# Kernel optimization log

Measured on AMD Instinct MI355X. Metric: run time of the kernel, lower is better.

## Reference

```python
import jax, jax.numpy as jnp
import numpy as np

N = 1000   # node count forced by fc1_1 in_features=1680 (see shape derivation)
E = 8000   # edges, avg degree ~8
F_IN = 6   # node feature dim (first 3 = pos, zeroed in forward)


def setup_inputs() -> dict:
    key = jax.random.key(0)
    ks = jax.random.split(key, 24)
    f = lambda k, s, sc=1.0: jax.random.normal(k, s, dtype=jnp.float32) * sc
    inp = {
        "x": f(ks[0], (N, F_IN)),
        "edge_index": jax.random.randint(ks[1], (2, E), 0, N, dtype=jnp.int64),
        # GCNConv weights (xavier-ish scale)
        "W1": f(ks[2], (F_IN, 32), 0.4), "b1": jnp.zeros((32,), jnp.float32),
        "W2": f(ks[3], (32, 32), 0.18), "b2": jnp.zeros((32,), jnp.float32),
        # Conv2d kernels, OIHW
        "k1": f(ks[4], (3, 1, 3, 2), 0.3), "kb1": jnp.zeros((3,), jnp.float32),
        "k2": f(ks[5], (6, 3, 3, 2), 0.2), "kb2": jnp.zeros((6,), jnp.float32),
        "k3": f(ks[6], (3, 6, 3, 2), 0.2), "kb3": jnp.zeros((3,), jnp.float32),
        "k4": f(ks[7], (1, 3, 3, 2), 0.2), "kb4": jnp.zeros((1,), jnp.float32),
        # FC head (torch Linear layout: [out, in])
        "fw1": f(ks[8], (1024, 1680), 0.02), "fb1": jnp.zeros((1024,), jnp.float32),
        "fw2": f(ks[9], (1024, 1024), 0.03), "fb2": jnp.zeros((1024,), jnp.float32),
        "fw3": f(ks[10], (64, 1024), 0.03), "fb3": jnp.zeros((64,), jnp.float32),
    }
    return inp


def _conv2d(x, w, b):
    out = jax.lax.conv_general_dilated(
        x, w, window_strides=(1, 1), padding="VALID",
        dimension_numbers=("NCHW", "OIHW", "NCHW"))
    return out + b[None, :, None, None]


def _maxpool2(x):  # MaxPool2d((2,1), stride=(2,1))
    return jax.lax.reduce_window(x, -jnp.inf, jax.lax.max,
                                 (1, 1, 2, 1), (1, 1, 2, 1), "VALID")


def reference(x, edge_index, W1, b1, W2, b2, k1, kb1, k2, kb2, k3, kb3, k4, kb4,
              fw1, fb1, fw2, fb2, fw3, fb3):
    num_nodes = x.shape[0]
    # forward zeroes the first 3 features (positions)
    x = x.at[:, :3].set(0.0)

    loop = jnp.arange(num_nodes)
    row = jnp.concatenate([edge_index[0], loop])
    col = jnp.concatenate([edge_index[1], loop])
    deg = jnp.zeros((num_nodes,), x.dtype).at[col].add(1.0)
    dinv = jnp.where(deg > 0, jax.lax.rsqrt(deg), 0.0)
    norm = (dinv[row] * dinv[col])[:, None]  # [E+N, 1]

    def gcn(h, W, b):
        hw = h @ W                                   # [N, 32]
        msg = hw[row] * norm                         # gather + scale
        return jax.ops.segment_sum(msg, col, num_segments=num_nodes) + b

    leaky = lambda v: jnp.where(v > 0, v, 0.2 * v)   # LeakyReLU(0.2)
    h = leaky(gcn(x, W1, b1))
    h = leaky(gcn(h, W2, b2))                        # [N, 32]

    img = h[None, None]                              # [1, 1, N, 32]
    img = _maxpool2(jax.nn.relu(_conv2d(img, k1, kb1)))   # [1,3,499,31]
    img = _maxpool2(jax.nn.relu(_conv2d(img, k2, kb2)))   # [1,6,248,30]
    img = _maxpool2(jax.nn.relu(_conv2d(img, k3, kb3)))   # [1,3,123,29]
    img = _maxpool2(jax.nn.relu(_conv2d(img, k4, kb4)))   # [1,1,60,28]

    v = img.reshape(-1)                              # [1680]
    v = v @ fw1.T + fb1                              # no activation between FCs (as in source)
    v = v @ fw2.T + fb2
    v = v @ fw3.T + fb3                              # [64]
    return v
```

## Files before the change

kernel.cpp:

```cpp
#include <hip/hip_runtime.h>

#define LEAKY(v) ((v) > 0.0f ? (v) : 0.2f * (v))

__global__ void k1_prep(const float* __restrict__ x, const int* __restrict__ col,
                        const float* __restrict__ W1, float* __restrict__ deg,
                        float* __restrict__ aggs ,
                        float* __restrict__ xw, int n, int E) {
    int tid = blockIdx.x * blockDim.x + threadIdx.x;
    int NT = gridDim.x * blockDim.x;
    for (int i = tid; i < 2 * n * 32; i += NT) aggs[i] = 0.0f;
    for (int e = tid; e < E; e += NT) atomicAdd(&deg[col[e]], 1.0f);
    for (int t = tid; t < n * 32; t += NT) {
        int j = t & 31, nn = t >> 5;
        xw[t] = x[nn*6+3] * W1[96+j]
              + x[nn*6+4] * W1[128+j]
              + x[nn*6+5] * W1[160+j];
    }
}

__global__ void k_scatter(const float* __restrict__ xw, const float* __restrict__ deg,
                          const int* __restrict__ row, const int* __restrict__ col,
                          float* __restrict__ agg, int E, int n) {
    int tid = blockIdx.x * blockDim.x + threadIdx.x;
    int total = (E + n) * 32;
    if (tid >= total) return;
    int e = tid >> 5, j = tid & 31;
    int r, c; float nrm;
    if (e < E) {
        r = row[e]; c = col[e];
        nrm = (1.0f / sqrtf(deg[r] + 1.0f)) * (1.0f / sqrtf(deg[c] + 1.0f));
    } else {
        r = c = e - E;
        nrm = 1.0f / (deg[r] + 1.0f);
    }
    atomicAdd(&agg[c * 32 + j], xw[r * 32 + j] * nrm);
}

__global__ void k3_xw2(const float* __restrict__ agg1, const float* __restrict__ b1,
                       const float* __restrict__ W2, float* __restrict__ xw, int n) {
    int tid = blockIdx.x * blockDim.x + threadIdx.x;
    if (tid >= n * 32) return;
    int j = tid & 31, nn = tid >> 5;
    const float* a = agg1 + nn * 32;
    float s = 0.0f;
#pragma unroll
    for (int f = 0; f < 32; ++f) {
        float v = a[f] + b1[f];
        v = LEAKY(v);
        s += v * W2[f * 32 + j];
    }
    xw[tid] = s;
}

__global__ void k5_conv1(const float* __restrict__ h2, const float* __restrict__ b2,
                         const float* __restrict__ w, const float* __restrict__ bias,
                         float* __restrict__ out) {
    const int Hp = 499, Wo = 31, total = 3 * Hp * Wo;
    int t0 = blockIdx.x * blockDim.x + threadIdx.x;
    if (t0 >= total) return;
    int ow = t0 % Wo; int t = t0 / Wo; int oh = t % Hp; int co = t / Hp;
    const float* ip = h2 + (2 * oh) * 32 + ow;
    float vals[4][2];
#pragma unroll
    for (int r = 0; r < 4; ++r)
#pragma unroll
        for (int cx = 0; cx < 2; ++cx) {
            float v = ip[r * 32 + cx] + b2[ow + cx];
            vals[r][cx] = LEAKY(v);
        }
    const float* wp = w + co * 6;
    float a0 = vals[0][0]*wp[0] + vals[0][1]*wp[1] + vals[1][0]*wp[2]
             + vals[1][1]*wp[3] + vals[2][0]*wp[4] + vals[2][1]*wp[5];
    float a1 = vals[1][0]*wp[0] + vals[1][1]*wp[1] + vals[2][0]*wp[2]
             + vals[2][1]*wp[3] + vals[3][0]*wp[4] + vals[3][1]*wp[5];
    float m = fmaxf(a0, a1) + bias[co];
    out[t0] = fmaxf(m, 0.0f);
}

__global__ void k6_conv2(const float* __restrict__ in, const float* __restrict__ w,
                         const float* __restrict__ bias, float* __restrict__ out) {
    const int CI = 3, Hin = 499, Win = 31, Hp = 248, Wo = 30, total = 6 * Hp * Wo;
    int t0 = blockIdx.x * blockDim.x + threadIdx.x;
    if (t0 >= total) return;
    int ow = t0 % Wo; int t = t0 / Wo; int oh = t % Hp; int co = t / Hp;
    float a0 = 0.0f, a1 = 0.0f;
#pragma unroll
    for (int ci = 0; ci < CI; ++ci) {
        const float* q = in + (ci * Hin + 2 * oh) * Win + ow;
        const float* wp = w + (co * CI + ci) * 6;
        float r00 = q[0],     r01 = q[1];
        float r10 = q[Win],   r11 = q[Win+1];
        float r20 = q[2*Win], r21 = q[2*Win+1];
        float r30 = q[3*Win], r31 = q[3*Win+1];
        a0 += r00*wp[0] + r01*wp[1] + r10*wp[2] + r11*wp[3] + r20*wp[4] + r21*wp[5];
        a1 += r10*wp[0] + r11*wp[1] + r20*wp[2] + r21*wp[3] + r30*wp[4] + r31*wp[5];
    }
    float m = fmaxf(a0, a1) + bias[co];
    out[t0] = fmaxf(m, 0.0f);
}

__global__ void k7_conv3(const float* __restrict__ in, const float* __restrict__ w,
                         const float* __restrict__ bias, float* __restrict__ out) {
    const int CI = 6, Hin = 248, Win = 30, Hp = 123, Wo = 29, total = 3 * Hp * Wo;
    int t0 = blockIdx.x * blockDim.x + threadIdx.x;
    if (t0 >= total) return;
    int ow = t0 % Wo; int t = t0 / Wo; int oh = t % Hp; int co = t / Hp;
    float a0 = 0.0f, a1 = 0.0f;
#pragma unroll
    for (int ci = 0; ci < CI; ++ci) {
        const float* q = in + (ci * Hin + 2 * oh) * Win + ow;
        const float* wp = w + (co * CI + ci) * 6;
        float r00 = q[0],     r01 = q[1];
        float r10 = q[Win],   r11 = q[Win+1];
        float r20 = q[2*Win], r21 = q[2*Win+1];
        float r30 = q[3*Win], r31 = q[3*Win+1];
        a0 += r00*wp[0] + r01*wp[1] + r10*wp[2] + r11*wp[3] + r20*wp[4] + r21*wp[5];
        a1 += r10*wp[0] + r11*wp[1] + r20*wp[2] + r21*wp[3] + r30*wp[4] + r31*wp[5];
    }
    float m = fmaxf(a0, a1) + bias[co];
    out[t0] = fmaxf(m, 0.0f);
}

__global__ __launch_bounds__(256) void k8_conv4_fc1(
        const float* __restrict__ c3, const float* __restrict__ k4,
        const float* __restrict__ kb4, const float* __restrict__ fw1,
        const float* __restrict__ fb1, float* __restrict__ f1) {
    __shared__ __align__(16) float lc4[1680];
    const int Hin = 123, Win = 29, Wo = 28;
    float kb = kb4[0];
    for (int t0 = (int)threadIdx.x; t0 < 1680; t0 += 256) {
        int ow = t0 % Wo; int oh = t0 / Wo;
        float a0 = 0.0f, a1 = 0.0f;
#pragma unroll
        for (int ci = 0; ci < 3; ++ci) {
            const float* q = c3 + (ci * Hin + 2 * oh) * Win + ow;
            const float* wp = k4 + ci * 6;
            float r00 = q[0],     r01 = q[1];
            float r10 = q[Win],   r11 = q[Win+1];
            float r20 = q[2*Win], r21 = q[2*Win+1];
            float r30 = q[3*Win], r31 = q[3*Win+1];
            a0 += r00*wp[0] + r01*wp[1] + r10*wp[2] + r11*wp[3] + r20*wp[4] + r21*wp[5];
            a1 += r10*wp[0] + r11*wp[1] + r20*wp[2] + r21*wp[3] + r30*wp[4] + r31*wp[5];
        }
        float m = fmaxf(a0, a1) + kb;
        lc4[t0] = fmaxf(m, 0.0f);
    }
    __syncthreads();
    int wv = threadIdx.x >> 6, lane = threadIdx.x & 63;
    int o = blockIdx.x * 4 + wv;
    const float4* wr = (const float4*)(fw1 + (size_t)o * 1680);
    const float4* vv = (const float4*)lc4;
    float s = 0.0f;
    for (int i = lane; i < 420; i += 64) {
        float4 a = vv[i], ww = wr[i];
        s += a.x*ww.x + a.y*ww.y + a.z*ww.z + a.w*ww.w;
    }
#pragma unroll
    for (int off = 32; off > 0; off >>= 1) s += __shfl_down(s, off, 64);
    if (lane == 0) f1[o] = s + fb1[o];
}

__global__ __launch_bounds__(256) void k_fc1024(const float* __restrict__ v,
                                                const float* __restrict__ w,
                                                const float* __restrict__ b,
                                                float* __restrict__ out) {
    int wv = threadIdx.x >> 6, lane = threadIdx.x & 63;
    int o = blockIdx.x * 4 + wv;
    const float4* wr = (const float4*)(w + (size_t)o * 1024);
    const float4* vv = (const float4*)v;
    float s = 0.0f;
#pragma unroll
    for (int i = 0; i < 4; ++i) {
        float4 a = vv[lane + 64*i], ww = wr[lane + 64*i];
        s += a.x*ww.x + a.y*ww.y + a.z*ww.z + a.w*ww.w;
    }
#pragma unroll
    for (int off = 32; off > 0; off >>= 1) s += __shfl_down(s, off, 64);
    if (lane == 0) out[o] = s + b[o];
}

extern "C" void kernel_launch(void* const* d_in, const int* in_sizes, int n_in,
                              void* d_out, int out_size, void* d_ws, size_t ws_size,
                              hipStream_t stream) {
    const float* x   = (const float*)d_in[0];
    const int*   ei  = (const int*)d_in[1];
    const float* W1  = (const float*)d_in[2];
    const float* b1  = (const float*)d_in[3];
    const float* W2  = (const float*)d_in[4];
    const float* b2  = (const float*)d_in[5];
    const float* k1  = (const float*)d_in[6];
    const float* kb1 = (const float*)d_in[7];
    const float* k2  = (const float*)d_in[8];
    const float* kb2 = (const float*)d_in[9];
    const float* k3  = (const float*)d_in[10];
    const float* kb3 = (const float*)d_in[11];
    const float* k4  = (const float*)d_in[12];
    const float* kb4 = (const float*)d_in[13];
    const float* fw1 = (const float*)d_in[14];
    const float* fb1 = (const float*)d_in[15];
    const float* fw2 = (const float*)d_in[16];
    const float* fb2 = (const float*)d_in[17];
    const float* fw3 = (const float*)d_in[18];
    const float* fb3 = (const float*)d_in[19];

    int n = in_sizes[0] / 6;
    int E = in_sizes[1] / 2;
    const int* row = ei;
    const int* col = ei + E;

    float* ws   = (float*)d_ws;
    float* deg  = ws;
    float* agg1 = ws + 1024;
    float* agg2 = agg1 + 32000;
    float* xw   = agg2 + 32000;
    float* c1   = xw + 32000;
    float* c2   = c1 + 46407;
    float* c3   = c2 + 44640;
    float* f1   = c3 + 10704;
    float* f2   = f1 + 1024;

    const int B = 256;

    hipMemsetAsync(deg, 0, n * sizeof(float), stream);
    k1_prep<<<256, B, 0, stream>>>(x, col, W1, deg, agg1, xw, n, E);
    int st = (E + n) * 32;
    k_scatter<<<(st + B - 1) / B, B, 0, stream>>>(xw, deg, row, col, agg1, E, n);
    k3_xw2<<<(n * 32 + B - 1) / B, B, 0, stream>>>(agg1, b1, W2, xw, n);
    k_scatter<<<(st + B - 1) / B, B, 0, stream>>>(xw, deg, row, col, agg2, E, n);
    k5_conv1<<<(3 * 499 * 31 + B - 1) / B, B, 0, stream>>>(agg2, b2, k1, kb1, c1);
    k6_conv2<<<(6 * 248 * 30 + B - 1) / B, B, 0, stream>>>(c1, k2, kb2, c2);
    k7_conv3<<<(3 * 123 * 29 + B - 1) / B, B, 0, stream>>>(c2, k3, kb3, c3);
    k8_conv4_fc1<<<256, B, 0, stream>>>(c3, k4, kb4, fw1, fb1, f1);
    k_fc1024<<<256, B, 0, stream>>>(f1, fw2, fb2, f2);
    k_fc1024<<<16, B, 0, stream>>>(f2, fw3, fb3, (float*)d_out);
}
```

Measured before the change: 134.1 us.

## Fuse conv1-3 into one tiled kernel and count degrees in shared memory

Conv1, conv2 and conv3 (each with relu and maxpool) are merged into one kernel. Each of 123 blocks computes one conv3 output row, recomputing the conv1 and conv2 halo rows it needs in shared memory. This removes two launches and the global c1/c2 intermediates. Degree counting moves to block 0 using shared-memory atomics, so the separate memset launch goes away. The trade-off is a little redundant conv1/conv2 work on overlapping rows and a serial degree pass in a single block.

```diff
diff --git a/kernel.cpp b/kernel.cpp
--- a/kernel.cpp
+++ b/kernel.cpp
@@ -2,19 +2,28 @@
 
 #define LEAKY(v) ((v) > 0.0f ? (v) : 0.2f * (v))
 
-__global__ void k1_prep(const float* __restrict__ x, const int* __restrict__ col,
-                        const float* __restrict__ W1, float* __restrict__ deg,
-                        float* __restrict__ aggs ,
-                        float* __restrict__ xw, int n, int E) {
-    int tid = blockIdx.x * blockDim.x + threadIdx.x;
-    int NT = gridDim.x * blockDim.x;
-    for (int i = tid; i < 2 * n * 32; i += NT) aggs[i] = 0.0f;
-    for (int e = tid; e < E; e += NT) atomicAdd(&deg[col[e]], 1.0f);
-    for (int t = tid; t < n * 32; t += NT) {
-        int j = t & 31, nn = t >> 5;
-        xw[t] = x[nn*6+3] * W1[96+j]
-              + x[nn*6+4] * W1[128+j]
-              + x[nn*6+5] * W1[160+j];
+__global__ __launch_bounds__(256) void k1_prep(
+        const float* __restrict__ x, const int* __restrict__ col,
+        const float* __restrict__ W1, float* __restrict__ deg,
+        float* __restrict__ aggs ,
+        float* __restrict__ xw, int n, int E) {
+    if (blockIdx.x == 0) {
+        __shared__ float sdeg[1024];
+        for (int i = threadIdx.x; i < n; i += 256) sdeg[i] = 0.0f;
+        __syncthreads();
+        for (int e = threadIdx.x; e < E; e += 256) atomicAdd(&sdeg[col[e]], 1.0f);
+        __syncthreads();
+        for (int i = threadIdx.x; i < n; i += 256) deg[i] = sdeg[i];
+    } else {
+        int tid = (blockIdx.x - 1) * 256 + threadIdx.x;
+        int NT = (gridDim.x - 1) * 256;
+        for (int i = tid; i < 2 * n * 32; i += NT) aggs[i] = 0.0f;
+        for (int t = tid; t < n * 32; t += NT) {
+            int j = t & 31, nn = t >> 5;
+            xw[t] = x[nn*6+3] * W1[96+j]
+                  + x[nn*6+4] * W1[128+j]
+                  + x[nn*6+5] * W1[160+j];
+        }
     }
 }
 
@@ -52,76 +61,75 @@
     xw[tid] = s;
 }
 
-__global__ void k5_conv1(const float* __restrict__ h2, const float* __restrict__ b2,
-                         const float* __restrict__ w, const float* __restrict__ bias,
-                         float* __restrict__ out) {
-    const int Hp = 499, Wo = 31, total = 3 * Hp * Wo;
-    int t0 = blockIdx.x * blockDim.x + threadIdx.x;
-    if (t0 >= total) return;
-    int ow = t0 % Wo; int t = t0 / Wo; int oh = t % Hp; int co = t / Hp;
-    const float* ip = h2 + (2 * oh) * 32 + ow;
-    float vals[4][2];
-#pragma unroll
-    for (int r = 0; r < 4; ++r)
-#pragma unroll
-        for (int cx = 0; cx < 2; ++cx) {
-            float v = ip[r * 32 + cx] + b2[ow + cx];
-            vals[r][cx] = LEAKY(v);
-        }
-    const float* wp = w + co * 6;
-    float a0 = vals[0][0]*wp[0] + vals[0][1]*wp[1] + vals[1][0]*wp[2]
-             + vals[1][1]*wp[3] + vals[2][0]*wp[4] + vals[2][1]*wp[5];
-    float a1 = vals[1][0]*wp[0] + vals[1][1]*wp[1] + vals[2][0]*wp[2]
-             + vals[2][1]*wp[3] + vals[3][0]*wp[4] + vals[3][1]*wp[5];
-    float m = fmaxf(a0, a1) + bias[co];
-    out[t0] = fmaxf(m, 0.0f);
-}
-
-__global__ void k6_conv2(const float* __restrict__ in, const float* __restrict__ w,
-                         const float* __restrict__ bias, float* __restrict__ out) {
-    const int CI = 3, Hin = 499, Win = 31, Hp = 248, Wo = 30, total = 6 * Hp * Wo;
-    int t0 = blockIdx.x * blockDim.x + threadIdx.x;
-    if (t0 >= total) return;
-    int ow = t0 % Wo; int t = t0 / Wo; int oh = t % Hp; int co = t / Hp;
-    float a0 = 0.0f, a1 = 0.0f;
-#pragma unroll
-    for (int ci = 0; ci < CI; ++ci) {
-        const float* q = in + (ci * Hin + 2 * oh) * Win + ow;
-        const float* wp = w + (co * CI + ci) * 6;
-        float r00 = q[0],     r01 = q[1];
-        float r10 = q[Win],   r11 = q[Win+1];
-        float r20 = q[2*Win], r21 = q[2*Win+1];
-        float r30 = q[3*Win], r31 = q[3*Win+1];
-        a0 += r00*wp[0] + r01*wp[1] + r10*wp[2] + r11*wp[3] + r20*wp[4] + r21*wp[5];
-        a1 += r10*wp[0] + r11*wp[1] + r20*wp[2] + r21*wp[3] + r30*wp[4] + r31*wp[5];
-    }
-    float m = fmaxf(a0, a1) + bias[co];
-    out[t0] = fmaxf(m, 0.0f);
-}
-
-__global__ void k7_conv3(const float* __restrict__ in, const float* __restrict__ w,
-                         const float* __restrict__ bias, float* __restrict__ out) {
-    const int CI = 6, Hin = 248, Win = 30, Hp = 123, Wo = 29, total = 3 * Hp * Wo;
-    int t0 = blockIdx.x * blockDim.x + threadIdx.x;
-    if (t0 >= total) return;
-    int ow = t0 % Wo; int t = t0 / Wo; int oh = t % Hp; int co = t / Hp;
-    float a0 = 0.0f, a1 = 0.0f;
-#pragma unroll
-    for (int ci = 0; ci < CI; ++ci) {
-        const float* q = in + (ci * Hin + 2 * oh) * Win + ow;
-        const float* wp = w + (co * CI + ci) * 6;
-        float r00 = q[0],     r01 = q[1];
-        float r10 = q[Win],   r11 = q[Win+1];
-        float r20 = q[2*Win], r21 = q[2*Win+1];
-        float r30 = q[3*Win], r31 = q[3*Win+1];
-        a0 += r00*wp[0] + r01*wp[1] + r10*wp[2] + r11*wp[3] + r20*wp[4] + r21*wp[5];
-        a1 += r10*wp[0] + r11*wp[1] + r20*wp[2] + r21*wp[3] + r30*wp[4] + r31*wp[5];
-    }
-    float m = fmaxf(a0, a1) + bias[co];
-    out[t0] = fmaxf(m, 0.0f);
-}
-
-__global__ __launch_bounds__(256) void k8_conv4_fc1(
+__global__ __launch_bounds__(256) void k5_conv123(
+        const float* __restrict__ h2, const float* __restrict__ b2,
+        const float* __restrict__ k1w, const float* __restrict__ kb1,
+        const float* __restrict__ k2w, const float* __restrict__ kb2,
+        const float* __restrict__ k3w, const float* __restrict__ kb3,
+        float* __restrict__ c3) {
+    __shared__ float lc1[10 * 3 * 31];
+    __shared__ float lc2[4 * 6 * 30];
+    const int b = blockIdx.x;
+
+    for (int t = threadIdx.x; t < 10 * 3 * 31; t += 256) {
+        int col_ = t % 31; int tt = t / 31; int co = tt % 3; int rl = tt / 3;
+        int oh1 = 4 * b + rl;
+        const float* ip = h2 + (2 * oh1) * 32 + col_;
+        float v[4][2];
+#pragma unroll
+        for (int r = 0; r < 4; ++r)
+#pragma unroll
+            for (int cx = 0; cx < 2; ++cx) {
+                float u = ip[r * 32 + cx] + b2[col_ + cx];
+                v[r][cx] = LEAKY(u);
+            }
+        const float* wp = k1w + co * 6;
+        float a0 = v[0][0]*wp[0] + v[0][1]*wp[1] + v[1][0]*wp[2]
+                 + v[1][1]*wp[3] + v[2][0]*wp[4] + v[2][1]*wp[5];
+        float a1 = v[1][0]*wp[0] + v[1][1]*wp[1] + v[2][0]*wp[2]
+                 + v[2][1]*wp[3] + v[3][0]*wp[4] + v[3][1]*wp[5];
+        float m = fmaxf(a0, a1) + kb1[co];
+        lc1[t] = fmaxf(m, 0.0f);
+    }
+    __syncthreads();
+
+    for (int t = threadIdx.x; t < 4 * 6 * 30; t += 256) {
+        int col_ = t % 30; int tt = t / 30; int co = tt % 6; int rl2 = tt / 6;
+        float a0 = 0.0f, a1 = 0.0f;
+#pragma unroll
+        for (int ci = 0; ci < 3; ++ci) {
+            const float* wp = k2w + (co * 3 + ci) * 6;
+            const float* q0 = lc1 + ((2*rl2 + 0) * 3 + ci) * 31 + col_;
+            const float* q1 = lc1 + ((2*rl2 + 1) * 3 + ci) * 31 + col_;
+            const float* q2 = lc1 + ((2*rl2 + 2) * 3 + ci) * 31 + col_;
+            const float* q3 = lc1 + ((2*rl2 + 3) * 3 + ci) * 31 + col_;
+            a0 += q0[0]*wp[0] + q0[1]*wp[1] + q1[0]*wp[2] + q1[1]*wp[3] + q2[0]*wp[4] + q2[1]*wp[5];
+            a1 += q1[0]*wp[0] + q1[1]*wp[1] + q2[0]*wp[2] + q2[1]*wp[3] + q3[0]*wp[4] + q3[1]*wp[5];
+        }
+        float m = fmaxf(a0, a1) + kb2[co];
+        lc2[(rl2 * 6 + co) * 30 + col_] = fmaxf(m, 0.0f);
+    }
+    __syncthreads();
+
+    for (int t = threadIdx.x; t < 3 * 29; t += 256) {
+        int col_ = t % 29; int co = t / 29;
+        float a0 = 0.0f, a1 = 0.0f;
+#pragma unroll
+        for (int ci = 0; ci < 6; ++ci) {
+            const float* wp = k3w + (co * 6 + ci) * 6;
+            const float* q0 = lc2 + (0 * 6 + ci) * 30 + col_;
+            const float* q1 = lc2 + (1 * 6 + ci) * 30 + col_;
+            const float* q2 = lc2 + (2 * 6 + ci) * 30 + col_;
+            const float* q3 = lc2 + (3 * 6 + ci) * 30 + col_;
+            a0 += q0[0]*wp[0] + q0[1]*wp[1] + q1[0]*wp[2] + q1[1]*wp[3] + q2[0]*wp[4] + q2[1]*wp[5];
+            a1 += q1[0]*wp[0] + q1[1]*wp[1] + q2[0]*wp[2] + q2[1]*wp[3] + q3[0]*wp[4] + q3[1]*wp[5];
+        }
+        float m = fmaxf(a0, a1) + kb3[co];
+        c3[(co * 123 + b) * 29 + col_] = fmaxf(m, 0.0f);
+    }
+}
+
+__global__ __launch_bounds__(256) void k6_conv4_fc1(
         const float* __restrict__ c3, const float* __restrict__ k4,
         const float* __restrict__ kb4, const float* __restrict__ fw1,
         const float* __restrict__ fb1, float* __restrict__ f1) {
@@ -213,24 +221,19 @@
     float* agg1 = ws + 1024;
     float* agg2 = agg1 + 32000;
     float* xw   = agg2 + 32000;
-    float* c1   = xw + 32000;
-    float* c2   = c1 + 46407;
-    float* c3   = c2 + 44640;
+    float* c3   = xw + 32000;
     float* f1   = c3 + 10704;
     float* f2   = f1 + 1024;
 
     const int B = 256;
 
-    hipMemsetAsync(deg, 0, n * sizeof(float), stream);
     k1_prep<<<256, B, 0, stream>>>(x, col, W1, deg, agg1, xw, n, E);
     int st = (E + n) * 32;
     k_scatter<<<(st + B - 1) / B, B, 0, stream>>>(xw, deg, row, col, agg1, E, n);
     k3_xw2<<<(n * 32 + B - 1) / B, B, 0, stream>>>(agg1, b1, W2, xw, n);
     k_scatter<<<(st + B - 1) / B, B, 0, stream>>>(xw, deg, row, col, agg2, E, n);
-    k5_conv1<<<(3 * 499 * 31 + B - 1) / B, B, 0, stream>>>(agg2, b2, k1, kb1, c1);
-    k6_conv2<<<(6 * 248 * 30 + B - 1) / B, B, 0, stream>>>(c1, k2, kb2, c2);
-    k7_conv3<<<(3 * 123 * 29 + B - 1) / B, B, 0, stream>>>(c2, k3, kb3, c3);
-    k8_conv4_fc1<<<256, B, 0, stream>>>(c3, k4, kb4, fw1, fb1, f1);
+    k5_conv123<<<123, B, 0, stream>>>(agg2, b2, k1, kb1, k2, kb2, k3, kb3, c3);
+    k6_conv4_fc1<<<256, B, 0, stream>>>(c3, k4, kb4, fw1, fb1, f1);
     k_fc1024<<<256, B, 0, stream>>>(f1, fw2, fb2, f2);
     k_fc1024<<<16, B, 0, stream>>>(f2, fw3, fb3, (float*)d_out);
 }
```

Result: slower. 139.4 us (+3.9%).
